# Kernel optimization log

Measured on AMD Instinct MI355X. Metric: run time of the kernel, lower is better.

## Reference

```python
import jax, jax.numpy as jnp
import numpy as np

BN_EPS = 1e-3  # Keras BatchNormalization default epsilon

def setup_inputs() -> dict:
    key = jax.random.key(0)
    ks = jax.random.split(key, 6)
    B, H, W, C = 8, 128, 128, 128
    s = 0.05  # small init scale for weights
    return {
        "x1": jax.random.normal(ks[0], (B, H, W, C), jnp.float32),
        "x2": jax.random.normal(ks[1], (B, H, W, C), jnp.float32),
        "Wq": jax.random.normal(ks[2], (C, C), jnp.float32) * s,
        "Wk": jax.random.normal(ks[3], (C, C), jnp.float32) * s,
        "Wv": jax.random.normal(ks[4], (C, C), jnp.float32) * s,
        "Ws": jax.random.normal(ks[5], (C, C), jnp.float32) * s,
        "bs": jnp.zeros((C,), jnp.float32),
        "scale": jnp.ones((1,), jnp.float32),   # layers.Attention use_scale=True, init 1
        "gamma": jnp.ones((C,), jnp.float32),
        "beta": jnp.zeros((C,), jnp.float32),
        "mu": jnp.zeros((C,), jnp.float32),
        "var": jnp.ones((C,), jnp.float32),
    }


def reference(x1, x2, Wq, Wk, Wv, Ws, bs, scale, gamma, beta, mu, var):
    # x1, x2: [B,H,W,C].  1x1 convs with relu == per-pixel channel matmul.
    q = jax.nn.relu(jnp.einsum('bhwc,cd->bhwd', x1, Wq))  # [B,H,W,C]
    k = jax.nn.relu(jnp.einsum('bhwc,cd->bhwd', x1, Wk))
    v = jax.nn.relu(jnp.einsum('bhwc,cd->bhwd', x2, Wv))
    # After transpose [0,3,1,2], Keras Attention batches over (B,C):
    # seq axis = H (rows), feature dim = W (cols). Fold the transposes into einsum.
    scores = scale[0] * jnp.einsum('bhwc,bgwc->bchg', q, k)  # [B,C,H,H]
    attn = jax.nn.softmax(scores, axis=-1)
    # attn @ v over row axis g, then implicit transpose back to NHWC.
    o = jnp.einsum('bchg,bgwc->bhwc', attn, v)  # [B,H,W,C]
    # sigmoid 1x1 conv (with bias), then inference-mode BatchNorm.
    g = jax.nn.sigmoid(jnp.einsum('bhwc,cd->bhwd', o, Ws) + bs)
    g = gamma * (g - mu) * jax.lax.rsqrt(var + BN_EPS) + beta
    # gated residual
    return x1 + x2 * g
```

## Files before the change

### kernel.cpp

```cpp
#include <hip/hip_runtime.h>

typedef unsigned int u32;
typedef unsigned short u16;
typedef u16 u16x4 __attribute__((ext_vector_type(4)));
typedef u16 u16x8 __attribute__((ext_vector_type(8)));
typedef __bf16 bf16x8 __attribute__((ext_vector_type(8)));
typedef float f32x4 __attribute__((ext_vector_type(4)));

#define LDK 136
#define MFMA(a, b, c) __builtin_amdgcn_mfma_f32_16x16x32_bf16(a, b, c, 0, 0, 0)

__device__ __forceinline__ u16 f2b(float f) {
  u32 u = __builtin_bit_cast(u32, f);
  u = (u + 0x7fffu + ((u >> 16) & 1u)) >> 16;
  return (u16)u;
}
__device__ __forceinline__ float b2f(u16 h) {
  u32 u = ((u32)h) << 16;
  return __builtin_bit_cast(float, u);
}

__global__ void wprep(const float* __restrict__ Wq, const float* __restrict__ Wk,
                      const float* __restrict__ Wv, const float* __restrict__ Ws,
                      u16* __restrict__ wT) {
  const float* srcs[4] = {Wq, Wk, Wv, Ws};
  const float* s = srcs[blockIdx.x];
  u16* d = wT + (size_t)blockIdx.x * 16384;
  for (int idx = threadIdx.x; idx < 16384; idx += 256) {
    int i = idx >> 7, j = idx & 127;
    d[j * 128 + i] = f2b(s[idx]);
  }
}

__global__ __launch_bounds__(256, 4)
void qkv_kernel(const float* __restrict__ x1, const float* __restrict__ x2,
                const u16* __restrict__ wT,
                u16* __restrict__ q_t, u16* __restrict__ k_t, u16* __restrict__ v_t) {
  __shared__ u16 Xs[128 * LDK];

  const int t = threadIdx.x;
  const int bh = blockIdx.x;
  const int m = blockIdx.y;
  const int b = bh >> 7, h = bh & 127;
  const size_t pixbase = (size_t)bh * 16384;
  const size_t obase = (size_t)b * 2097152 + (size_t)h * 128;

  const float* xin = (m == 2) ? x2 : x1;
  u16* dst = (m == 0) ? q_t : (m == 1) ? k_t : v_t;

  const int lane = t & 63, wave = t >> 6;
  const int lrow = lane & 15, lq = lane >> 4;
  const int nstrip = wave * 32;

  const u16* wb = wT + (size_t)m * 16384;
  bf16x8 w0[4], w1[4];
#pragma unroll
  for (int kk = 0; kk < 4; ++kk) {
    int ko = kk * 32 + lq * 8;
    w0[kk] = *(const bf16x8*)&wb[(nstrip + lrow) * 128 + ko];
    w1[kk] = *(const bf16x8*)&wb[(nstrip + 16 + lrow) * 128 + ko];
  }

#pragma unroll
  for (int j = 0; j < 8; ++j) {
    int lin = j * 256 + t;
    int w = lin >> 4, c0 = (lin & 15) << 3;
    f32x4 a0 = *(const f32x4*)&xin[pixbase + lin * 8];
    f32x4 a1 = *(const f32x4*)&xin[pixbase + lin * 8 + 4];
    u16x8 p;
#pragma unroll
    for (int i = 0; i < 4; ++i) { p[i] = f2b(a0[i]); p[4 + i] = f2b(a1[i]); }
    *(u16x8*)&Xs[w * LDK + c0] = p;
  }
  __syncthreads();

  f32x4 acc[8][2];
#pragma unroll
  for (int mt = 0; mt < 8; ++mt) {
    acc[mt][0] = (f32x4){0.f, 0.f, 0.f, 0.f};
    acc[mt][1] = (f32x4){0.f, 0.f, 0.f, 0.f};
  }
#pragma unroll
  for (int kk = 0; kk < 4; ++kk) {
    int ko = kk * 32 + lq * 8;
#pragma unroll
    for (int mt = 0; mt < 8; ++mt) {
      bf16x8 a = *(const bf16x8*)&Xs[(mt * 16 + lrow) * LDK + ko];
      acc[mt][0] = MFMA(a, w0[kk], acc[mt][0]);
      acc[mt][1] = MFMA(a, w1[kk], acc[mt][1]);
    }
  }

#pragma unroll
  for (int mt = 0; mt < 8; ++mt) {
    int w0i = mt * 16 + lq * 4;
#pragma unroll
    for (int nt = 0; nt < 2; ++nt) {
      int c = nstrip + nt * 16 + lrow;
      u16x4 p;
#pragma unroll
      for (int r = 0; r < 4; ++r) p[r] = f2b(fmaxf(acc[mt][nt][r], 0.f));
      *(u16x4*)&dst[obase + (size_t)c * 16384 + w0i] = p;
    }
  }
}

__global__ __launch_bounds__(256, 2)
void attn_kernel(u16* __restrict__ q_t, const u16* __restrict__ k_t,
                 const u16* __restrict__ v_t, const float* __restrict__ scale_p) {
  __shared__ u16 Ks[128 * LDK];
  __shared__ u16 Ps[128 * LDK];

  const int t = threadIdx.x;
  const size_t base = (size_t)blockIdx.x * 16384;

  const int lane = t & 63, wave = t >> 6;
  const int lrow = lane & 15, lq = lane >> 4;
  const int hstrip = wave * 32;
  const float scl = scale_p[0];

  bf16x8 q0[4], q1[4];
#pragma unroll
  for (int kk = 0; kk < 4; ++kk) {
    int ko = kk * 32 + lq * 8;
    q0[kk] = *(const bf16x8*)&q_t[base + (hstrip + lrow) * 128 + ko];
    q1[kk] = *(const bf16x8*)&q_t[base + (hstrip + 16 + lrow) * 128 + ko];
  }
  const int g0 = (t & 15) * 8, w0v = (t >> 4) * 8;
  u16x8 vv[8];
#pragma unroll
  for (int i = 0; i < 8; ++i)
    vv[i] = *(const u16x8*)&v_t[base + (g0 + i) * 128 + w0v];
#pragma unroll
  for (int j = 0; j < 8; ++j) {
    int lin = j * 256 + t;
    int r = lin >> 4, c0 = (lin & 15) << 3;
    *(u16x8*)&Ks[r * LDK + c0] = *(const u16x8*)&k_t[base + lin * 8];
  }
  __syncthreads();

  f32x4 acc[8][2];
#pragma unroll
  for (int mt = 0; mt < 8; ++mt) {
    acc[mt][0] = (f32x4){0.f, 0.f, 0.f, 0.f};
    acc[mt][1] = (f32x4){0.f, 0.f, 0.f, 0.f};
  }
#pragma unroll
  for (int kk = 0; kk < 4; ++kk) {
    int ko = kk * 32 + lq * 8;
#pragma unroll
    for (int mt = 0; mt < 8; ++mt) {
      bf16x8 a = *(const bf16x8*)&Ks[(mt * 16 + lrow) * LDK + ko];
      acc[mt][0] = MFMA(a, q0[kk], acc[mt][0]);
      acc[mt][1] = MFMA(a, q1[kk], acc[mt][1]);
    }
  }

  float inv[2];
#pragma unroll
  for (int nt = 0; nt < 2; ++nt) {
    float mx = -1e30f;
#pragma unroll
    for (int mt = 0; mt < 8; ++mt)
#pragma unroll
      for (int r = 0; r < 4; ++r) {
        acc[mt][nt][r] *= scl;
        mx = fmaxf(mx, acc[mt][nt][r]);
      }
    mx = fmaxf(mx, __shfl_xor(mx, 16));
    mx = fmaxf(mx, __shfl_xor(mx, 32));
    float s = 0.f;
#pragma unroll
    for (int mt = 0; mt < 8; ++mt)
#pragma unroll
      for (int r = 0; r < 4; ++r) {
        float e = __expf(acc[mt][nt][r] - mx);
        acc[mt][nt][r] = e;
        s += e;
      }
    s += __shfl_xor(s, 16);
    s += __shfl_xor(s, 32);
    inv[nt] = 1.f / s;
  }
  __syncthreads();

#pragma unroll
  for (int j = 0; j < 8; ++j) {
    u16x8 tv;
#pragma unroll
    for (int i = 0; i < 8; ++i) tv[i] = vv[i][j];
    *(u16x8*)&Ks[(w0v + j) * LDK + g0] = tv;
  }
#pragma unroll
  for (int mt = 0; mt < 8; ++mt) {
    int gg0 = mt * 16 + lq * 4;
#pragma unroll
    for (int nt = 0; nt < 2; ++nt) {
      int hh = hstrip + nt * 16 + lrow;
      u16x4 p;
#pragma unroll
      for (int r = 0; r < 4; ++r) p[r] = f2b(acc[mt][nt][r] * inv[nt]);
      *(u16x4*)&Ps[hh * LDK + gg0] = p;
    }
  }
  __syncthreads();

#pragma unroll
  for (int kk = 0; kk < 4; ++kk) {
    int ko = kk * 32 + lq * 8;
    bf16x8 b0 = *(const bf16x8*)&Ps[(hstrip + lrow) * LDK + ko];
    bf16x8 b1 = *(const bf16x8*)&Ps[(hstrip + 16 + lrow) * LDK + ko];
    if (kk == 0) {
#pragma unroll
      for (int mt = 0; mt < 8; ++mt) {
        acc[mt][0] = (f32x4){0.f, 0.f, 0.f, 0.f};
        acc[mt][1] = (f32x4){0.f, 0.f, 0.f, 0.f};
      }
    }
#pragma unroll
    for (int mt = 0; mt < 8; ++mt) {
      bf16x8 a = *(const bf16x8*)&Ks[(mt * 16 + lrow) * LDK + ko];
      acc[mt][0] = MFMA(a, b0, acc[mt][0]);
      acc[mt][1] = MFMA(a, b1, acc[mt][1]);
    }
  }
#pragma unroll
  for (int mt = 0; mt < 8; ++mt) {
    int w0i = mt * 16 + lq * 4;
#pragma unroll
    for (int nt = 0; nt < 2; ++nt) {
      int hh = hstrip + nt * 16 + lrow;
      u16x4 p;
#pragma unroll
      for (int r = 0; r < 4; ++r) p[r] = f2b(acc[mt][nt][r]);
      *(u16x4*)&q_t[base + hh * 128 + w0i] = p;
    }
  }
}

__global__ __launch_bounds__(256, 4)
void final_kernel(const u16* __restrict__ o_t, const u16* __restrict__ wsT,
                  const float* __restrict__ x1, const float* __restrict__ x2,
                  const float* __restrict__ bs, const float* __restrict__ gamma,
                  const float* __restrict__ beta, const float* __restrict__ mu,
                  const float* __restrict__ var, float* __restrict__ out) {
  __shared__ u16 Os[128 * LDK];
  __shared__ float bnA[128], bnB[128], bsf[128];

  const int t = threadIdx.x;
  const int bh = blockIdx.x;
  const int b = bh >> 7, h = bh & 127;
  const size_t obase = (size_t)b * 2097152 + (size_t)h * 128;
  const size_t pixbase = (size_t)bh * 16384;

  if (t < 128) {
    float a = gamma[t] * rsqrtf(var[t] + 1e-3f);
    bnA[t] = a;
    bnB[t] = beta[t] - mu[t] * a;
    bsf[t] = bs[t];
  }
  {
    int c0 = (t & 15) * 8, w0 = (t >> 4) * 8;
    u16 ov[8][8];
#pragma unroll
    for (int i = 0; i < 8; ++i)
      *(u16x8*)&ov[i][0] = *(const u16x8*)&o_t[obase + (size_t)(c0 + i) * 16384 + w0];
#pragma unroll
    for (int j = 0; j < 8; ++j) {
      u16x8 tv;
#pragma unroll
      for (int i = 0; i < 8; ++i) tv[i] = ov[i][j];
      *(u16x8*)&Os[(w0 + j) * LDK + c0] = tv;
    }
  }
  __syncthreads();

  const int lane = t & 63, wave = t >> 6;
  const int lrow = lane & 15, lq = lane >> 4;
  const int wstrip = wave * 32;

  f32x4 acc[8][2];
#pragma unroll
  for (int mt = 0; mt < 8; ++mt) {
    acc[mt][0] = (f32x4){0.f, 0.f, 0.f, 0.f};
    acc[mt][1] = (f32x4){0.f, 0.f, 0.f, 0.f};
  }
#pragma unroll
  for (int kk = 0; kk < 4; ++kk) {
    int ko = kk * 32 + lq * 8;
    bf16x8 b0 = *(const bf16x8*)&Os[(wstrip + lrow) * LDK + ko];
    bf16x8 b1 = *(const bf16x8*)&Os[(wstrip + 16 + lrow) * LDK + ko];
#pragma unroll
    for (int mt = 0; mt < 8; ++mt) {
      bf16x8 a = *(const bf16x8*)&wsT[(mt * 16 + lrow) * 128 + ko];
      acc[mt][0] = MFMA(a, b0, acc[mt][0]);
      acc[mt][1] = MFMA(a, b1, acc[mt][1]);
    }
  }
  __syncthreads();

#pragma unroll
  for (int mt = 0; mt < 8; ++mt) {
    int d0 = mt * 16 + lq * 4;
#pragma unroll
    for (int nt = 0; nt < 2; ++nt) {
      int w = wstrip + nt * 16 + lrow;
      u16x4 p;
#pragma unroll
      for (int r = 0; r < 4; ++r) {
        int d = d0 + r;
        float sv = acc[mt][nt][r] + bsf[d];
        float sg = 1.f / (1.f + __expf(-sv));
        p[r] = f2b(bnA[d] * sg + bnB[d]);
      }
      *(u16x4*)&Os[w * LDK + d0] = p;
    }
  }
  __syncthreads();

  {
    int w = t >> 1, d0 = (t & 1) * 64;
#pragma unroll
    for (int j = 0; j < 8; ++j) {
      int d = d0 + j * 8;
      u16x8 g8 = *(const u16x8*)&Os[w * LDK + d];
      f32x4 a0 = *(const f32x4*)&x1[pixbase + w * 128 + d];
      f32x4 a1 = *(const f32x4*)&x1[pixbase + w * 128 + d + 4];
      f32x4 c0v = *(const f32x4*)&x2[pixbase + w * 128 + d];
      f32x4 c1v = *(const f32x4*)&x2[pixbase + w * 128 + d + 4];
      f32x4 r0, r1;
#pragma unroll
      for (int i = 0; i < 4; ++i) {
        r0[i] = a0[i] + c0v[i] * b2f(g8[i]);
        r1[i] = a1[i] + c1v[i] * b2f(g8[4 + i]);
      }
      *(f32x4*)&out[pixbase + w * 128 + d] = r0;
      *(f32x4*)&out[pixbase + w * 128 + d + 4] = r1;
    }
  }
}

extern "C" void kernel_launch(void* const* d_in, const int* in_sizes, int n_in,
                              void* d_out, int out_size, void* d_ws, size_t ws_size,
                              hipStream_t stream) {
  const float* x1 = (const float*)d_in[0];
  const float* x2 = (const float*)d_in[1];
  const float* Wq = (const float*)d_in[2];
  const float* Wk = (const float*)d_in[3];
  const float* Wv = (const float*)d_in[4];
  const float* Ws = (const float*)d_in[5];
  const float* bs = (const float*)d_in[6];
  const float* scale = (const float*)d_in[7];
  const float* gamma = (const float*)d_in[8];
  const float* beta = (const float*)d_in[9];
  const float* mu = (const float*)d_in[10];
  const float* var = (const float*)d_in[11];
  float* outp = (float*)d_out;

  u16* q_t = (u16*)d_ws;
  u16* k_t = q_t + 16777216;
  u16* v_t = k_t + 16777216;
  u16* wT = v_t + 16777216;

  wprep<<<dim3(4), dim3(256), 0, stream>>>(Wq, Wk, Wv, Ws, wT);
  qkv_kernel<<<dim3(1024, 3), dim3(256), 0, stream>>>(x1, x2, wT, q_t, k_t, v_t);
  attn_kernel<<<dim3(1024), dim3(256), 0, stream>>>(q_t, k_t, v_t, scale);
  final_kernel<<<dim3(1024), dim3(256), 0, stream>>>(q_t, wT + 3 * 16384, x1, x2, bs,
                                                     gamma, beta, mu, var, outp);
}
```

Measured before the change: 343.9 us.

## Share x1 staging for Q and K projections; fuse gated residual epilogue

The QKV kernel now runs one block per (b,h) row, which stages x1 once into shared memory and computes both Q and K from it, then restages x2 for V. This removes the duplicate x1 read and bf16 conversion that the three-way grid split caused. In the final kernel, the sigmoid/BN gate and the residual are computed straight from MFMA accumulators. The gate is no longer rounded to bf16 and round-tripped through LDS, and two barriers go away, at the cost of less coalesced per-lane global loads and stores of x1, x2 and out. Each QKV block also does more serial work, so there is less parallelism per launch.

```diff
diff --git a/kernel.cpp b/kernel.cpp
--- a/kernel.cpp
+++ b/kernel.cpp
@@ -32,35 +32,9 @@
   }
 }
 
-__global__ __launch_bounds__(256, 4)
-void qkv_kernel(const float* __restrict__ x1, const float* __restrict__ x2,
-                const u16* __restrict__ wT,
-                u16* __restrict__ q_t, u16* __restrict__ k_t, u16* __restrict__ v_t) {
-  __shared__ u16 Xs[128 * LDK];
-
-  const int t = threadIdx.x;
-  const int bh = blockIdx.x;
-  const int m = blockIdx.y;
-  const int b = bh >> 7, h = bh & 127;
-  const size_t pixbase = (size_t)bh * 16384;
-  const size_t obase = (size_t)b * 2097152 + (size_t)h * 128;
-
-  const float* xin = (m == 2) ? x2 : x1;
-  u16* dst = (m == 0) ? q_t : (m == 1) ? k_t : v_t;
-
-  const int lane = t & 63, wave = t >> 6;
-  const int lrow = lane & 15, lq = lane >> 4;
-  const int nstrip = wave * 32;
-
-  const u16* wb = wT + (size_t)m * 16384;
-  bf16x8 w0[4], w1[4];
-#pragma unroll
-  for (int kk = 0; kk < 4; ++kk) {
-    int ko = kk * 32 + lq * 8;
-    w0[kk] = *(const bf16x8*)&wb[(nstrip + lrow) * 128 + ko];
-    w1[kk] = *(const bf16x8*)&wb[(nstrip + 16 + lrow) * 128 + ko];
-  }
-
+__device__ __forceinline__ void stage_x(u16* __restrict__ Xs,
+                                        const float* __restrict__ xin,
+                                        size_t pixbase, int t) {
 #pragma unroll
   for (int j = 0; j < 8; ++j) {
     int lin = j * 256 + t;
@@ -72,8 +46,19 @@
     for (int i = 0; i < 4; ++i) { p[i] = f2b(a0[i]); p[4 + i] = f2b(a1[i]); }
     *(u16x8*)&Xs[w * LDK + c0] = p;
   }
-  __syncthreads();
-
+}
+
+__device__ __forceinline__ void gemm_relu_store(const u16* __restrict__ Xs,
+                                                const u16* __restrict__ wb,
+                                                u16* __restrict__ dst, size_t obase,
+                                                int lrow, int lq, int nstrip) {
+  bf16x8 w0[4], w1[4];
+#pragma unroll
+  for (int kk = 0; kk < 4; ++kk) {
+    int ko = kk * 32 + lq * 8;
+    w0[kk] = *(const bf16x8*)&wb[(nstrip + lrow) * 128 + ko];
+    w1[kk] = *(const bf16x8*)&wb[(nstrip + 16 + lrow) * 128 + ko];
+  }
   f32x4 acc[8][2];
 #pragma unroll
   for (int mt = 0; mt < 8; ++mt) {
@@ -90,7 +75,6 @@
       acc[mt][1] = MFMA(a, w1[kk], acc[mt][1]);
     }
   }
-
 #pragma unroll
   for (int mt = 0; mt < 8; ++mt) {
     int w0i = mt * 16 + lq * 4;
@@ -103,6 +87,32 @@
       *(u16x4*)&dst[obase + (size_t)c * 16384 + w0i] = p;
     }
   }
+}
+
+__global__ __launch_bounds__(256, 4)
+void qkv_kernel(const float* __restrict__ x1, const float* __restrict__ x2,
+                const u16* __restrict__ wT,
+                u16* __restrict__ q_t, u16* __restrict__ k_t, u16* __restrict__ v_t) {
+  __shared__ u16 Xs[128 * LDK];
+
+  const int t = threadIdx.x;
+  const int bh = blockIdx.x;
+  const int b = bh >> 7, h = bh & 127;
+  const size_t pixbase = (size_t)bh * 16384;
+  const size_t obase = (size_t)b * 2097152 + (size_t)h * 128;
+
+  const int lane = t & 63, wave = t >> 6;
+  const int lrow = lane & 15, lq = lane >> 4;
+  const int nstrip = wave * 32;
+
+  stage_x(Xs, x1, pixbase, t);
+  __syncthreads();
+  gemm_relu_store(Xs, wT, q_t, obase, lrow, lq, nstrip);
+  gemm_relu_store(Xs, wT + 16384, k_t, obase, lrow, lq, nstrip);
+  __syncthreads();
+  stage_x(Xs, x2, pixbase, t);
+  __syncthreads();
+  gemm_relu_store(Xs, wT + 2 * 16384, v_t, obase, lrow, lq, nstrip);
 }
 
 __global__ __launch_bounds__(256, 2)
@@ -297,45 +307,28 @@
       acc[mt][1] = MFMA(a, b1, acc[mt][1]);
     }
   }
-  __syncthreads();
 
 #pragma unroll
   for (int mt = 0; mt < 8; ++mt) {
     int d0 = mt * 16 + lq * 4;
+    f32x4 A4 = *(const f32x4*)&bnA[d0];
+    f32x4 B4 = *(const f32x4*)&bnB[d0];
+    f32x4 S4 = *(const f32x4*)&bsf[d0];
 #pragma unroll
     for (int nt = 0; nt < 2; ++nt) {
       int w = wstrip + nt * 16 + lrow;
-      u16x4 p;
-#pragma unroll
-      for (int r = 0; r < 4; ++r) {
-        int d = d0 + r;
-        float sv = acc[mt][nt][r] + bsf[d];
+      size_t off = pixbase + (size_t)w * 128 + d0;
+      f32x4 a1v = *(const f32x4*)&x1[off];
+      f32x4 a2v = *(const f32x4*)&x2[off];
+      f32x4 r;
+#pragma unroll
+      for (int r4 = 0; r4 < 4; ++r4) {
+        float sv = acc[mt][nt][r4] + S4[r4];
         float sg = 1.f / (1.f + __expf(-sv));
-        p[r] = f2b(bnA[d] * sg + bnB[d]);
+        float g = A4[r4] * sg + B4[r4];
+        r[r4] = a1v[r4] + a2v[r4] * g;
       }
-      *(u16x4*)&Os[w * LDK + d0] = p;
-    }
-  }
-  __syncthreads();
-
-  {
-    int w = t >> 1, d0 = (t & 1) * 64;
-#pragma unroll
-    for (int j = 0; j < 8; ++j) {
-      int d = d0 + j * 8;
-      u16x8 g8 = *(const u16x8*)&Os[w * LDK + d];
-      f32x4 a0 = *(const f32x4*)&x1[pixbase + w * 128 + d];
-      f32x4 a1 = *(const f32x4*)&x1[pixbase + w * 128 + d + 4];
-      f32x4 c0v = *(const f32x4*)&x2[pixbase + w * 128 + d];
-      f32x4 c1v = *(const f32x4*)&x2[pixbase + w * 128 + d + 4];
-      f32x4 r0, r1;
-#pragma unroll
-      for (int i = 0; i < 4; ++i) {
-        r0[i] = a0[i] + c0v[i] * b2f(g8[i]);
-        r1[i] = a1[i] + c1v[i] * b2f(g8[4 + i]);
-      }
-      *(f32x4*)&out[pixbase + w * 128 + d] = r0;
-      *(f32x4*)&out[pixbase + w * 128 + d + 4] = r1;
+      *(f32x4*)&out[off] = r;
     }
   }
 }
@@ -363,7 +356,7 @@
   u16* wT = v_t + 16777216;
 
   wprep<<<dim3(4), dim3(256), 0, stream>>>(Wq, Wk, Wv, Ws, wT);
-  qkv_kernel<<<dim3(1024, 3), dim3(256), 0, stream>>>(x1, x2, wT, q_t, k_t, v_t);
+  qkv_kernel<<<dim3(1024), dim3(256), 0, stream>>>(x1, x2, wT, q_t, k_t, v_t);
   attn_kernel<<<dim3(1024), dim3(256), 0, stream>>>(q_t, k_t, v_t, scale);
   final_kernel<<<dim3(1024), dim3(256), 0, stream>>>(q_t, wT + 3 * 16384, x1, x2, bs,
                                                      gamma, beta, mu, var, outp);
```

After: 413.5 us. 20.3% more time.
